# Optimization experiments

Measured on AMD Instinct MI355X. Metric: run time of the kernel, lower is better.

## Reference

```python
import jax, jax.numpy as jnp
import numpy as np

E = 256      # embed_dim
K = 8        # kNN neighbors (hard-coded in module)
B = 64       # num cells (samples)
P = 512      # objects per cell (equal segments)
N = B * P
NUM_CLASSES = 31  # 30 known + <unk> (padding idx 0)


def _normalize(x, axis=-1):
    n = jnp.linalg.norm(x, axis=axis, keepdims=True)
    return x / jnp.clip(n, 1e-12, None)


def _mlp2(x, W1, b1, W2, b2):
    # get_mlp([d_in, 64/E, d_out]): Linear-ReLU-Linear
    return jax.nn.relu(x @ W1 + b1) @ W2 + b2


def setup_inputs() -> dict:
    key = jax.random.key(0)
    ks = jax.random.split(key, 32)

    def w(k, shape, s=0.05):
        return (jax.random.normal(k, shape, jnp.float32) * s).astype(jnp.float32)

    class_table = w(ks[0], (NUM_CLASSES, E))
    class_table = class_table.at[0].set(0.0)  # padding_idx=0

    inp = {
        # learned params
        "class_table": class_table,
        "colorW1": w(ks[1], (3, 64)), "colorb1": jnp.zeros((64,), jnp.float32),
        "colorW2": w(ks[2], (64, E)), "colorb2": jnp.zeros((E,), jnp.float32),
        "posW1": w(ks[3], (3, 64)), "posb1": jnp.zeros((64,), jnp.float32),
        "posW2": w(ks[4], (64, E)), "posb2": jnp.zeros((E,), jnp.float32),
        "mergeW": w(ks[5], (3 * E, E)), "mergeb": jnp.zeros((E,), jnp.float32),
        # DynamicEdgeConv mlp: Linear(2E,E)-ReLU-BN(E)-Linear(E,E)
        "gW1": w(ks[6], (2 * E, E)), "gb1": jnp.zeros((E,), jnp.float32),
        "g_gamma": jnp.ones((E,), jnp.float32), "g_beta": jnp.zeros((E,), jnp.float32),
        "gW2": w(ks[7], (E, E)), "gb2": jnp.zeros((E,), jnp.float32),
        # final lin: Linear(E,E)-ReLU-Linear(E,E)
        "lW1": w(ks[8], (E, E)), "lb1": jnp.zeros((E,), jnp.float32),
        "lW2": w(ks[9], (E, E)), "lb2": jnp.zeros((E,), jnp.float32),
        # forward inputs
        "positions": jax.random.normal(ks[10], (N, 3), jnp.float32),
        "colors": jax.random.uniform(ks[11], (N, 3), jnp.float32),
        "class_indices": jax.random.randint(ks[12], (N,), 0, NUM_CLASSES, jnp.int64),
        "num_samples": B,
    }
    return inp


def reference(class_table, colorW1, colorb1, colorW2, colorb2,
              posW1, posb1, posW2, posb2, mergeW, mergeb,
              gW1, gb1, g_gamma, g_beta, gW2, gb2,
              lW1, lb1, lW2, lb2,
              positions, colors, class_indices, num_samples):
    # --- per-object embeddings, each L2-normalized, then merged ---
    ce = _normalize(class_table[class_indices])                         # [N,E]
    co = _normalize(_mlp2(colors, colorW1, colorb1, colorW2, colorb2))  # [N,E]
    pe = _normalize(_mlp2(positions, posW1, posb1, posW2, posb2))       # [N,E]
    emb = jnp.concatenate([ce, co, pe], axis=-1) @ mergeW + mergeb      # [N,E]

    # --- DynamicEdgeConv (variation 0): per-sample kNN in feature space ---
    x = emb.reshape(num_samples, -1, E)                                 # [B,P,E]
    sq = jnp.sum(x * x, axis=-1)                                        # [B,P]
    dist = sq[:, :, None] + sq[:, None, :] - 2.0 * jnp.einsum('bpe,bqe->bpq', x, x)
    _, idx = jax.lax.top_k(-dist, K)                                    # [B,P,K] (incl. self)

    x_nb = jax.vmap(lambda xb, ib: xb[ib])(x, idx)                      # [B,P,K,E]
    x_i = jnp.broadcast_to(x[:, :, None, :], x_nb.shape)
    msg_in = jnp.concatenate([x_i, x_nb - x_i], axis=-1)                # [B,P,K,2E]
    h = jax.nn.relu(msg_in @ gW1 + gb1)
    h = h * g_gamma + g_beta          # BatchNorm1d eval mode (running mean 0, var 1)
    h = h @ gW2 + gb2                                                   # [B,P,K,E]
    x1 = jnp.max(h, axis=2)                                             # max aggr -> [B,P,E]

    # --- global max pool over objects, final MLP, L2 normalize ---
    pooled = jnp.max(x1, axis=1)                                        # [B,E]
    out = _mlp2(pooled, lW1, lb1, lW2, lb2)
    return _normalize(out, axis=-1)
```

## Files before the change

kernel.cpp:

```cpp
#include <hip/hip_runtime.h>

#define EDIM 256
#define KNN 8
#define NB 64
#define NP 512
#define NTOT (NB * NP)

typedef short s16x8 __attribute__((ext_vector_type(8)));
typedef float f32x4 __attribute__((ext_vector_type(4)));
typedef float f32x16 __attribute__((ext_vector_type(16)));
typedef unsigned short ushort;
typedef unsigned long long u64;

__device__ __forceinline__ ushort f2b(float f) {
    unsigned u = __float_as_uint(f);
    u = (u + 0x7fffu + ((u >> 16) & 1u)) >> 16;
    return (ushort)u;
}
__device__ __forceinline__ float b2f(ushort h) {
    return __uint_as_float(((unsigned)h) << 16);
}
__device__ __forceinline__ void split2(float x, ushort& h, ushort& l) {
    h = f2b(x);
    l = f2b(x - b2f(h));
}

__device__ __forceinline__ unsigned fkey(float f) {
    const unsigned b = __float_as_uint(f);
    return (b & 0x80000000u) ? ~b : (b | 0x80000000u);
}

__device__ __forceinline__ void ins8(u64* k, u64 x) {
    #pragma unroll
    for (int j = 7; j >= 1; --j)
        k[j] = (x < k[j - 1]) ? k[j - 1] : ((x < k[j]) ? x : k[j]);
    k[0] = (x < k[0]) ? x : k[0];
}

__device__ __forceinline__ void gload16(const ushort* g, ushort* l) {
    __builtin_amdgcn_global_load_lds(
        (const __attribute__((address_space(1))) void*)g,
        (__attribute__((address_space(3))) void*)l, 16, 0, 0);
}

__global__ __launch_bounds__(256)
void k_prep(const float* __restrict__ gW1, const float* __restrict__ gW2,
            const float* __restrict__ g_gamma, const float* __restrict__ g_beta,
            const float* __restrict__ gb2,
            const float* __restrict__ cW2, const float* __restrict__ pW2,
            const float* __restrict__ cb2, const float* __restrict__ pb2,
            const float* __restrict__ mW, const float* __restrict__ ct,
            ushort* __restrict__ Wdh, ushort* __restrict__ Wdl,
            ushort* __restrict__ Wbh, ushort* __restrict__ Wbl,
            ushort* __restrict__ g2h, ushort* __restrict__ g2l,
            float* __restrict__ hb,
            ushort* __restrict__ cW2Th, ushort* __restrict__ cW2Tl,
            ushort* __restrict__ pW2Th, ushort* __restrict__ pW2Tl,
            ushort* __restrict__ WcTh, ushort* __restrict__ WcTl,
            ushort* __restrict__ WpTh, ushort* __restrict__ WpTl,
            float* __restrict__ cbM, float* __restrict__ pbM,
            float* __restrict__ classMn)
{
    __shared__ float ctn[256];
    __shared__ float red[4];
    const int bid = blockIdx.x, t = threadIdx.x;
    ushort h, l;

    if (bid < 897) {
        const int gid = bid * 256 + t;
        if (gid < 65536) {
            const int n = gid >> 8, k = gid & 255;
            split2(gW1[k * 256 + n] - gW1[(k + 256) * 256 + n], h, l);
            Wdh[gid] = h; Wdl[gid] = l;
        } else if (gid < 131072) {
            const int i = gid - 65536, n = i >> 8, k = i & 255;
            split2(gW1[(k + 256) * 256 + n], h, l);
            Wbh[i] = h; Wbl[i] = l;
        } else if (gid < 196608) {
            const int i = gid - 131072, n = i >> 8, k = i & 255;
            split2(g_gamma[k] * gW2[k * 256 + n], h, l);
            g2h[i] = h; g2l[i] = l;
        } else if (gid < 196864) {
            const int n = gid - 196608;
            float s = gb2[n];
            for (int k = 0; k < 256; ++k) s += g_beta[k] * gW2[k * 256 + n];
            hb[n] = s;
        } else if (gid < 213248) {
            const int i = gid - 196864, n = i >> 6, k = i & 63;
            split2(cW2[k * 256 + n], h, l);
            cW2Th[i] = h; cW2Tl[i] = l;
        } else if (gid < 229632) {
            const int i = gid - 213248, n = i >> 6, k = i & 63;
            split2(pW2[k * 256 + n], h, l);
            pW2Th[i] = h; pW2Tl[i] = l;
        }
        return;
    }
    if (bid < 1027) {
        const int gid = (bid - 897) * 256 + t;
        if (gid < 16384) {
            const int j = gid >> 8, n = gid & 255;
            float s = 0.f;
            for (int k = 0; k < 256; ++k) s += cW2[j * 256 + k] * mW[(256 + k) * 256 + n];
            split2(s, h, l);
            WcTh[n * 64 + j] = h; WcTl[n * 64 + j] = l;
        } else if (gid < 32768) {
            const int i = gid - 16384, j = i >> 8, n = i & 255;
            float s = 0.f;
            for (int k = 0; k < 256; ++k) s += pW2[j * 256 + k] * mW[(512 + k) * 256 + n];
            split2(s, h, l);
            WpTh[n * 64 + j] = h; WpTl[n * 64 + j] = l;
        } else if (gid < 33024) {
            const int n = gid - 32768;
            float s = 0.f;
            for (int k = 0; k < 256; ++k) s += cb2[k] * mW[(256 + k) * 256 + n];
            cbM[n] = s;
        } else if (gid < 33280) {
            const int n = gid - 33024;
            float s = 0.f;
            for (int k = 0; k < 256; ++k) s += pb2[k] * mW[(512 + k) * 256 + n];
            pbM[n] = s;
        }
        return;
    }
    {
        const int c = bid - 1027;
        const float v = ct[c * 256 + t];
        float ss = v * v;
        #pragma unroll
        for (int s = 32; s > 0; s >>= 1) ss += __shfl_down(ss, s, 64);
        if ((t & 63) == 0) red[t >> 6] = ss;
        __syncthreads();
        const float tot = red[0] + red[1] + red[2] + red[3];
        const float r = 1.f / fmaxf(sqrtf(tot), 1e-12f);
        ctn[t] = v * r;
        __syncthreads();
        float s = 0.f;
        for (int k = 0; k < 256; ++k) s += ctn[k] * mW[k * 256 + t];
        classMn[c * 256 + t] = s;
    }
}

__global__ __launch_bounds__(256)
void k_embed(const float* __restrict__ classMn,
             const float* __restrict__ cW1, const float* __restrict__ cb1,
             const float* __restrict__ cb2,
             const float* __restrict__ pW1, const float* __restrict__ pb1,
             const float* __restrict__ pb2,
             const float* __restrict__ mb,
             const ushort* __restrict__ cW2Th, const ushort* __restrict__ cW2Tl,
             const ushort* __restrict__ pW2Th, const ushort* __restrict__ pW2Tl,
             const ushort* __restrict__ WcTh, const ushort* __restrict__ WcTl,
             const ushort* __restrict__ WpTh, const ushort* __restrict__ WpTl,
             const float* __restrict__ cbM, const float* __restrict__ pbM,
             const float* __restrict__ positions, const float* __restrict__ colors,
             const int* __restrict__ cls, const int cstride,
             ushort* __restrict__ ehi, ushort* __restrict__ elo,
             float* __restrict__ sqn)
{
    __shared__ __align__(16) ushort Ahc[16 * 72];
    __shared__ __align__(16) ushort Alc[16 * 72];
    __shared__ __align__(16) ushort Ahp[16 * 72];
    __shared__ __align__(16) ushort Alp[16 * 72];
    __shared__ float sqc[16][4], sqp_[16][4], sqe[16][4];

    const int t = threadIdx.x, w = t >> 6, lane = t & 63;
    const int l15 = lane & 15, quad = lane >> 4;
    const int obase = blockIdx.x * 16;

    {
        const int o = lane >> 4;
        const int objl = w * 4 + o;
        const int gobj = obase + objl;
        const float c0 = colors[gobj * 3], c1 = colors[gobj * 3 + 1], c2 = colors[gobj * 3 + 2];
        const float q0 = positions[gobj * 3], q1 = positions[gobj * 3 + 1], q2 = positions[gobj * 3 + 2];
        const int u0 = (lane & 15) * 4;
        #pragma unroll
        for (int uu = 0; uu < 4; ++uu) {
            const int u = u0 + uu;
            const float hc = fmaxf(cb1[u] + c0 * cW1[u] + c1 * cW1[64 + u] + c2 * cW1[128 + u], 0.f);
            const float hp = fmaxf(pb1[u] + q0 * pW1[u] + q1 * pW1[64 + u] + q2 * pW1[128 + u], 0.f);
            ushort h, l;
            split2(hc, h, l); Ahc[objl * 72 + u] = h; Alc[objl * 72 + u] = l;
            split2(hp, h, l); Ahp[objl * 72 + u] = h; Alp[objl * 72 + u] = l;
        }
    }
    __syncthreads();

    f32x4 aco[4], ape[4];
    #pragma unroll
    for (int nt = 0; nt < 4; ++nt) { aco[nt] = (f32x4){0.f,0.f,0.f,0.f}; ape[nt] = (f32x4){0.f,0.f,0.f,0.f}; }

    #pragma unroll
    for (int kt = 0; kt < 2; ++kt) {
        const int ao = l15 * 72 + kt * 32 + quad * 8;
        const s16x8 ahc = *(const s16x8*)&Ahc[ao];
        const s16x8 alc = *(const s16x8*)&Alc[ao];
        const s16x8 ahp = *(const s16x8*)&Ahp[ao];
        const s16x8 alp = *(const s16x8*)&Alp[ao];
        #pragma unroll
        for (int nt = 0; nt < 4; ++nt) {
            const int n = w * 64 + nt * 16 + l15;
            const size_t bo = (size_t)n * 64 + kt * 32 + quad * 8;
            const s16x8 cbh = *(const s16x8*)(cW2Th + bo);
            const s16x8 cbl = *(const s16x8*)(cW2Tl + bo);
            const s16x8 pbh = *(const s16x8*)(pW2Th + bo);
            const s16x8 pbl = *(const s16x8*)(pW2Tl + bo);
            aco[nt] = __builtin_amdgcn_mfma_f32_16x16x32_bf16(ahc, cbh, aco[nt], 0, 0, 0);
            ape[nt] = __builtin_amdgcn_mfma_f32_16x16x32_bf16(ahp, pbh, ape[nt], 0, 0, 0);
            aco[nt] = __builtin_amdgcn_mfma_f32_16x16x32_bf16(alc, cbh, aco[nt], 0, 0, 0);
            ape[nt] = __builtin_amdgcn_mfma_f32_16x16x32_bf16(alp, pbh, ape[nt], 0, 0, 0);
            aco[nt] = __builtin_amdgcn_mfma_f32_16x16x32_bf16(ahc, cbl, aco[nt], 0, 0, 0);
            ape[nt] = __builtin_amdgcn_mfma_f32_16x16x32_bf16(ahp, pbl, ape[nt], 0, 0, 0);
        }
    }

    float sc[4] = {0.f,0.f,0.f,0.f}, sp[4] = {0.f,0.f,0.f,0.f};
    #pragma unroll
    for (int nt = 0; nt < 4; ++nt) {
        const int col = w * 64 + nt * 16 + l15;
        const float cbv = cb2[col], pbv = pb2[col];
        #pragma unroll
        for (int r = 0; r < 4; ++r) {
            const float co = aco[nt][r] + cbv;
            const float pe = ape[nt][r] + pbv;
            sc[r] += co * co;
            sp[r] += pe * pe;
        }
    }
    #pragma unroll
    for (int s = 8; s > 0; s >>= 1) {
        #pragma unroll
        for (int r = 0; r < 4; ++r) {
            sc[r] += __shfl_xor(sc[r], s, 64);
            sp[r] += __shfl_xor(sp[r], s, 64);
        }
    }
    if (l15 == 0) {
        #pragma unroll
        for (int r = 0; r < 4; ++r) { sqc[quad * 4 + r][w] = sc[r]; sqp_[quad * 4 + r][w] = sp[r]; }
    }
    __syncthreads();

    float rco[4], rpe[4];
    #pragma unroll
    for (int r = 0; r < 4; ++r) {
        const int row = quad * 4 + r;
        rco[r] = 1.f / fmaxf(sqrtf(sqc[row][0] + sqc[row][1] + sqc[row][2] + sqc[row][3]), 1e-12f);
        rpe[r] = 1.f / fmaxf(sqrtf(sqp_[row][0] + sqp_[row][1] + sqp_[row][2] + sqp_[row][3]), 1e-12f);
    }

    f32x4 ac[4], ap[4];
    #pragma unroll
    for (int nt = 0; nt < 4; ++nt) { ac[nt] = (f32x4){0.f,0.f,0.f,0.f}; ap[nt] = (f32x4){0.f,0.f,0.f,0.f}; }

    #pragma unroll
    for (int kt = 0; kt < 2; ++kt) {
        const int ao = l15 * 72 + kt * 32 + quad * 8;
        const s16x8 ahc = *(const s16x8*)&Ahc[ao];
        const s16x8 alc = *(const s16x8*)&Alc[ao];
        const s16x8 ahp = *(const s16x8*)&Ahp[ao];
        const s16x8 alp = *(const s16x8*)&Alp[ao];
        #pragma unroll
        for (int nt = 0; nt < 4; ++nt) {
            const int n = w * 64 + nt * 16 + l15;
            const size_t bo = (size_t)n * 64 + kt * 32 + quad * 8;
            const s16x8 cbh = *(const s16x8*)(WcTh + bo);
            const s16x8 cbl = *(const s16x8*)(WcTl + bo);
            const s16x8 pbh = *(const s16x8*)(WpTh + bo);
            const s16x8 pbl = *(const s16x8*)(WpTl + bo);
            ac[nt] = __builtin_amdgcn_mfma_f32_16x16x32_bf16(ahc, cbh, ac[nt], 0, 0, 0);
            ap[nt] = __builtin_amdgcn_mfma_f32_16x16x32_bf16(ahp, pbh, ap[nt], 0, 0, 0);
            ac[nt] = __builtin_amdgcn_mfma_f32_16x16x32_bf16(alc, cbh, ac[nt], 0, 0, 0);
            ap[nt] = __builtin_amdgcn_mfma_f32_16x16x32_bf16(alp, pbh, ap[nt], 0, 0, 0);
            ac[nt] = __builtin_amdgcn_mfma_f32_16x16x32_bf16(ahc, cbl, ac[nt], 0, 0, 0);
            ap[nt] = __builtin_amdgcn_mfma_f32_16x16x32_bf16(ahp, pbl, ap[nt], 0, 0, 0);
        }
    }

    int ci[4];
    #pragma unroll
    for (int r = 0; r < 4; ++r) {
        const int gobj = obase + quad * 4 + r;
        int c = cls[(size_t)gobj * cstride];
        if ((unsigned)c > 30u) c = 0;
        ci[r] = c;
    }

    float rp[4] = {0.f,0.f,0.f,0.f};
    #pragma unroll
    for (int nt = 0; nt < 4; ++nt) {
        const int col = w * 64 + nt * 16 + l15;
        const float mbv = mb[col], cbMv = cbM[col], pbMv = pbM[col];
        #pragma unroll
        for (int r = 0; r < 4; ++r) {
            const int row = quad * 4 + r;
            const float e = classMn[ci[r] * 256 + col]
                          + rco[r] * (ac[nt][r] + cbMv)
                          + rpe[r] * (ap[nt][r] + pbMv) + mbv;
            ushort h, l;
            split2(e, h, l);
            ehi[(size_t)(obase + row) * 256 + col] = h;
            elo[(size_t)(obase + row) * 256 + col] = l;
            rp[r] += e * e;
        }
    }
    #pragma unroll
    for (int s = 8; s > 0; s >>= 1) {
        #pragma unroll
        for (int r = 0; r < 4; ++r) rp[r] += __shfl_xor(rp[r], s, 64);
    }
    if (l15 == 0) {
        #pragma unroll
        for (int r = 0; r < 4; ++r) sqe[quad * 4 + r][w] = rp[r];
    }
    __syncthreads();
    if (t < 16) sqn[obase + t] = sqe[t][0] + sqe[t][1] + sqe[t][2] + sqe[t][3];
}

__global__ __launch_bounds__(256)
void k_gram(const ushort* __restrict__ ehi, const ushort* __restrict__ elo,
            const float* __restrict__ sqn, u64* __restrict__ cand)
{
    __shared__ __align__(16) ushort lds[2][4][4096];

    const int t = threadIdx.x, w = t >> 6, lane = t & 63;
    const int l15 = lane & 15, quad = lane >> 4;
    const int b = blockIdx.x;
    const int xcd = b & 7, rest = b >> 3;
    const int cell = xcd * 8 + rest / 10;
    const int tt = rest % 10;
    const int ti = (tt < 4) ? 0 : (tt < 7) ? 1 : (tt < 9) ? 2 : 3;
    const int tbase = (ti == 0) ? 0 : (ti == 1) ? 4 : (ti == 2) ? 7 : 9;
    const int tj = ti + (tt - tbase);
    const int p0 = ti * 128, q0 = tj * 128;
    const size_t cb = (size_t)cell * NP;
    const int diag = (ti == tj);
    const int wr = w >> 1, wc = w & 1;

    int srow[2], scol[2];
    #pragma unroll
    for (int i = 0; i < 2; ++i) {
        const int p = (w * 2 + i) * 64 + lane;
        const int row = p >> 2;
        srow[i] = row;
        scol[i] = ((p & 3) ^ ((row >> 1) & 3)) * 8;
    }

    #define STAGE(KT, D)                                                         \
    {                                                                            \
        const int kb_ = (KT) * 32;                                               \
        _Pragma("unroll")                                                        \
        for (int i = 0; i < 2; ++i) {                                            \
            const int ls_ = (w * 2 + i) * 512;               \
            const size_t ga_ = (cb + p0 + srow[i]) * 256 + kb_ + scol[i];        \
            gload16(ehi + ga_, &lds[D][0][ls_]);                                 \
            gload16(elo + ga_, &lds[D][1][ls_]);                                 \
            if (!diag) {                                                         \
                const size_t gq_ = (cb + q0 + srow[i]) * 256 + kb_ + scol[i];    \
                gload16(ehi + gq_, &lds[D][2][ls_]);                             \
                gload16(elo + gq_, &lds[D][3][ls_]);                             \
            }                                                                    \
        }                                                                        \
    }

    f32x4 acc[4][4];
    #pragma unroll
    for (int mt = 0; mt < 4; ++mt)
        #pragma unroll
        for (int nt = 0; nt < 4; ++nt) acc[mt][nt] = (f32x4){0.f, 0.f, 0.f, 0.f};

    const int bB = diag ? 0 : 2;

    STAGE(0, 0);
    __syncthreads();

    for (int kt = 0; kt < 8; ++kt) {
        const int cur = kt & 1;
        if (kt < 7) STAGE(kt + 1, cur ^ 1);

        s16x8 ah[4], al[4];
        #pragma unroll
        for (int mt = 0; mt < 4; ++mt) {
            const int r = wr * 64 + mt * 16 + l15;
            const int slot = 4 * r + (quad ^ ((r >> 1) & 3));
            ah[mt] = *(const s16x8*)&lds[cur][0][slot * 8];
            al[mt] = *(const s16x8*)&lds[cur][1][slot * 8];
        }
        #pragma unroll
        for (int nt = 0; nt < 4; ++nt) {
            const int rq = wc * 64 + nt * 16 + l15;
            const int slot = 4 * rq + (quad ^ ((rq >> 1) & 3));
            const s16x8 bh = *(const s16x8*)&lds[cur][bB][slot * 8];
            const s16x8 bl = *(const s16x8*)&lds[cur][bB + 1][slot * 8];
            #pragma unroll
            for (int mt = 0; mt < 4; ++mt) {
                acc[mt][nt] = __builtin_amdgcn_mfma_f32_16x16x32_bf16(ah[mt], bh, acc[mt][nt], 0, 0, 0);
                acc[mt][nt] = __builtin_amdgcn_mfma_f32_16x16x32_bf16(al[mt], bh, acc[mt][nt], 0, 0, 0);
                acc[mt][nt] = __builtin_amdgcn_mfma_f32_16x16x32_bf16(ah[mt], bl, acc[mt][nt], 0, 0, 0);
            }
        }
        __syncthreads();
    }
    #undef STAGE

    float sqp[4][4];
    #pragma unroll
    for (int mt = 0; mt < 4; ++mt)
        #pragma unroll
        for (int r = 0; r < 4; ++r)
            sqp[mt][r] = sqn[cb + p0 + wr * 64 + mt * 16 + quad * 4 + r];

    float* T = (float*)&lds[0][0][0];

    #pragma unroll
    for (int nt = 0; nt < 4; ++nt) {
        const int cq_l = wc * 64 + nt * 16 + l15;
        const float sq_q = sqn[cb + q0 + cq_l];
        #pragma unroll
        for (int mt = 0; mt < 4; ++mt) {
            #pragma unroll
            for (int r = 0; r < 4; ++r) {
                const int rp_l = wr * 64 + mt * 16 + quad * 4 + r;
                const float d = (sqp[mt][r] + sq_q) - 2.f * acc[mt][nt][r];
                T[rp_l * 128 + (cq_l ^ rp_l)] = d;
            }
        }
    }
    __syncthreads();

    {
        const int row = t >> 1, half = t & 1;

        u64 k8[8];
        #pragma unroll
        for (int j = 0; j < 8; ++j) k8[j] = ~0ull;
        for (int c = 0; c < 64; ++c) {
            const int cc = half * 64 + c;
            const float f = T[row * 128 + (cc ^ row)];
            ins8(k8, ((u64)fkey(f) << 32) | (unsigned)(q0 + cc));
        }
        {
            u64 part[8];
            #pragma unroll
            for (int j = 0; j < 8; ++j) part[j] = __shfl_xor(k8[j], 1, 64);
            #pragma unroll
            for (int j = 0; j < 8; ++j) ins8(k8, part[j]);
        }
        if (half == 0) {
            u64* cp = cand + ((size_t)(cb + p0 + row)) * 32 + tj * 8;
            #pragma unroll
            for (int j = 0; j < 8; ++j) cp[j] = k8[j];
        }

        if (!diag) {
            u64 q8[8];
            #pragma unroll
            for (int j = 0; j < 8; ++j) q8[j] = ~0ull;
            for (int c = 0; c < 64; ++c) {
                const int rr = half * 64 + c;
                const float f = T[rr * 128 + (row ^ rr)];
                ins8(q8, ((u64)fkey(f) << 32) | (unsigned)(p0 + rr));
            }
            {
                u64 part[8];
                #pragma unroll
                for (int j = 0; j < 8; ++j) part[j] = __shfl_xor(q8[j], 1, 64);
                #pragma unroll
                for (int j = 0; j < 8; ++j) ins8(q8, part[j]);
            }
            if (half == 0) {
                u64* cp = cand + ((size_t)(cb + q0 + row)) * 32 + ti * 8;
                #pragma unroll
                for (int j = 0; j < 8; ++j) cp[j] = q8[j];
            }
        }
    }
}

__global__ __launch_bounds__(256)
void k_nidx(const u64* __restrict__ cand, int* __restrict__ nidx)
{
    const int p = blockIdx.x * 256 + threadIdx.x;
    const u64* cp = cand + (size_t)p * 32;
    u64 k8[8];
    #pragma unroll
    for (int j = 0; j < 8; ++j) k8[j] = ~0ull;
    #pragma unroll
    for (int i = 0; i < 32; ++i) ins8(k8, cp[i]);
    const int hi = (p >> 9) << 9;
    #pragma unroll
    for (int r = 0; r < 8; ++r)
        nidx[(size_t)p * KNN + r] = hi | (int)(k8[r] & 0x1ffu);
}

__global__ __launch_bounds__(256)
void k_uv(const ushort* __restrict__ ehi, const ushort* __restrict__ elo,
          const ushort* __restrict__ Wdh, const ushort* __restrict__ Wbh,
          const float* __restrict__ gb1,
          float* __restrict__ u, float* __restrict__ v)
{
    (void)elo;
    __shared__ __align__(16) ushort lds[2][2048];

    const int t = threadIdx.x, w = t >> 6, lane = t & 63;
    const int l15 = lane & 15, quad = lane >> 4;
    const int isV = blockIdx.x >> 9;
    const int m0 = (blockIdx.x & 511) * 64;
    const ushort* Wh = isV ? Wbh : Wdh;
    float* out = isV ? v : u;
    const int mh = w & 1, ch = w >> 1;

    const int sp = w * 64 + lane;
    const int srow = sp >> 2;
    const int scol = ((sp & 3) ^ ((srow >> 1) & 3)) * 8;

    #define STAGE_UV(S, D)                                                       \
    {                                                                            \
        const size_t ga_ = (size_t)(m0 + srow) * 256 + (S) * 32 + scol;          \
        gload16(ehi + ga_, &lds[D][sp * 8]);                                     \
    }

    const int r0 = mh * 32 + l15, r1 = r0 + 16;
    const int slot0 = 4 * r0 + (quad ^ ((r0 >> 1) & 3));
    const int slot1 = 4 * r1 + (quad ^ ((r1 >> 1) & 3));

    f32x4 acc[2][8];
    #pragma unroll
    for (int mt = 0; mt < 2; ++mt)
        #pragma unroll
        for (int nt = 0; nt < 8; ++nt) acc[mt][nt] = (f32x4){0.f, 0.f, 0.f, 0.f};

    STAGE_UV(0, 0);
    __syncthreads();

    for (int s = 0; s < 8; ++s) {
        const int cur = s & 1;
        if (s < 7) STAGE_UV(s + 1, cur ^ 1);

        const s16x8 ah0 = *(const s16x8*)&lds[cur][slot0 * 8];
        const s16x8 ah1 = *(const s16x8*)&lds[cur][slot1 * 8];
        #pragma unroll
        for (int nt = 0; nt < 8; ++nt) {
            const int n = ch * 128 + nt * 16 + l15;
            const size_t bo = (size_t)n * 256 + s * 32 + quad * 8;
            const s16x8 bh = *(const s16x8*)(Wh + bo);
            acc[0][nt] = __builtin_amdgcn_mfma_f32_16x16x32_bf16(ah0, bh, acc[0][nt], 0, 0, 0);
            acc[1][nt] = __builtin_amdgcn_mfma_f32_16x16x32_bf16(ah1, bh, acc[1][nt], 0, 0, 0);
        }
        __syncthreads();
    }
    #undef STAGE_UV

    #pragma unroll
    for (int mt = 0; mt < 2; ++mt) {
        #pragma unroll
        for (int nt = 0; nt < 8; ++nt) {
            const int col = ch * 128 + nt * 16 + l15;
            const float bias = isV ? 0.f : gb1[col];
            #pragma unroll
            for (int r = 0; r < 4; ++r) {
                const int row = mh * 32 + mt * 16 + quad * 4 + r;
                out[(size_t)(m0 + row) * 256 + col] = acc[mt][nt][r] + bias;
            }
        }
    }
}

__global__ __launch_bounds__(512)
void k_edge(const float* __restrict__ u, const float* __restrict__ v,
            const int* __restrict__ nidx,
            const ushort* __restrict__ g2h,
            const float* __restrict__ hb,
            float* __restrict__ part)
{
    __shared__ ushort Abuf[2][2304];
    __shared__ float ustage[2048];

    const int t = threadIdx.x, w = t >> 6, lane = t & 63;
    const int l31 = lane & 31, kh = lane >> 5;

    const int b = blockIdx.x;
    const int xcd = b & 7, rest = b >> 3;
    const int cell = xcd * 8 + (rest >> 6);
    const int pl0 = cell * NP + (rest & 63) * 8;

    {
        const int pt = t >> 6, kk = (t & 63) * 4;
        *(float4*)&ustage[pt * 256 + kk] = *(const float4*)(u + (size_t)(pl0 + pt) * 256 + kk);
    }

    const int se = t >> 3, kq = t & 7;
    const int upt = se >> 3;
    int svrow = nidx[(size_t)(pl0 + upt) * KNN + (se & 7)];
    if ((unsigned)svrow >= (unsigned)NTOT) svrow = 0;

    __syncthreads();

    float4 vr[2];

    #define VLOAD(S)                                                             \
    {                                                                            \
        const int k0 = (S) * 32 + kq * 4;                                        \
        vr[(S) & 1] = *(const float4*)(v + (size_t)svrow * 256 + k0);            \
    }
    #define SPLITW(S, BUF)                                                       \
    {                                                                            \
        const int k0u = (S) * 32 + kq * 4;                                       \
        const float4 ua = *(const float4*)&ustage[upt * 256 + k0u];              \
        const float4 va = vr[(S) & 1];                                           \
        const float sv[4] = {                                                    \
            fmaxf(ua.x + va.x, 0.f), fmaxf(ua.y + va.y, 0.f),                    \
            fmaxf(ua.z + va.z, 0.f), fmaxf(ua.w + va.w, 0.f)};                   \
        union { uint2 q; ushort us[4]; } th;                                     \
        _Pragma("unroll")                                                        \
        for (int j = 0; j < 4; ++j) { th.us[j] = f2b(sv[j]); }                   \
        *(uint2*)&Abuf[BUF][se * 36 + kq * 4] = th.q;                            \
    }

    #define LDS_BARRIER()                                                        \
    {                                                                            \
        asm volatile("s_waitcnt lgkmcnt(0)" ::: "memory");                       \
        __builtin_amdgcn_s_barrier();                                            \
    }

    f32x16 acc[2];
    acc[0] = (f32x16)(0.0f);
    acc[1] = (f32x16)(0.0f);

    VLOAD(0); VLOAD(1);
    SPLITW(0, 0);

    #pragma unroll
    for (int s = 0; s < 8; ++s) {
        LDS_BARRIER();
        if (s < 7) {
            SPLITW(s + 1, (s + 1) & 1);
            if (s < 6) VLOAD(s + 2);
        }

        s16x8 ah[2][2];
        #pragma unroll
        for (int mt = 0; mt < 2; ++mt) {
            #pragma unroll
            for (int kc = 0; kc < 2; ++kc) {
                const int ao = (mt * 32 + l31) * 36 + kc * 16 + kh * 8;
                union { uint2 q[2]; s16x8 v8; } Th;
                Th.q[0] = *(const uint2*)&Abuf[s & 1][ao];
                Th.q[1] = *(const uint2*)&Abuf[s & 1][ao + 4];
                ah[mt][kc] = Th.v8;
            }
        }

        #pragma unroll
        for (int kc = 0; kc < 2; ++kc) {
            const int n = w * 32 + l31;
            const s16x8 bh = *(const s16x8*)(g2h + (size_t)n * 256 + s * 32 + kc * 16 + kh * 8);
            acc[0] = __builtin_amdgcn_mfma_f32_32x32x16_bf16(ah[0][kc], bh, acc[0], 0, 0, 0);
            acc[1] = __builtin_amdgcn_mfma_f32_32x32x16_bf16(ah[1][kc], bh, acc[1], 0, 0, 0);
        }
    }
    #undef VLOAD
    #undef SPLITW
    #undef LDS_BARRIER

    const int slot = rest & 63;
    {
        float rm = -3.4e38f;
        #pragma unroll
        for (int r = 0; r < 16; ++r)
            rm = fmaxf(rm, fmaxf(acc[0][r], acc[1][r]));
        rm = fmaxf(rm, __shfl_xor(rm, 32, 64));
        if (kh == 0) {
            const int col = w * 32 + l31;
            part[((size_t)cell * 64 + slot) * 256 + col] = rm + hb[col];
        }
    }
}

__global__ __launch_bounds__(256)
void k_final(const float* __restrict__ part,
             const float* __restrict__ lW1, const float* __restrict__ lb1,
             const float* __restrict__ lW2, const float* __restrict__ lb2,
             float* __restrict__ out)
{
    __shared__ float pooled[256];
    __shared__ float hid[256];
    __shared__ float red[4];

    const int b = blockIdx.x;
    const int t = threadIdx.x;

    float m = -3.4e38f;
    for (int s = 0; s < 64; ++s)
        m = fmaxf(m, part[((size_t)b * 64 + s) * 256 + t]);
    pooled[t] = m;
    __syncthreads();

    float h = lb1[t];
    for (int k = 0; k < 256; k += 4) {
        #pragma unroll
        for (int kk = 0; kk < 4; ++kk)
            h += pooled[k + kk] * lW1[(k + kk) * 256 + t];
    }
    hid[t] = fmaxf(h, 0.f);
    __syncthreads();

    float o = lb2[t];
    for (int k = 0; k < 256; k += 4) {
        #pragma unroll
        for (int kk = 0; kk < 4; ++kk)
            o += hid[k + kk] * lW2[(k + kk) * 256 + t];
    }

    float ss = o * o;
    #pragma unroll
    for (int s = 32; s > 0; s >>= 1) ss += __shfl_down(ss, s, 64);
    if ((t & 63) == 0) red[t >> 6] = ss;
    __syncthreads();
    const float tot = red[0] + red[1] + red[2] + red[3];
    const float rn = 1.f / fmaxf(sqrtf(tot), 1e-12f);
    out[b * 256 + t] = o * rn;
}

extern "C" void kernel_launch(void* const* d_in, const int* in_sizes, int n_in,
                              void* d_out, int out_size, void* d_ws, size_t ws_size,
                              hipStream_t stream)
{
    (void)n_in; (void)out_size; (void)ws_size;

    const float* class_table = (const float*)d_in[0];
    const float* cW1 = (const float*)d_in[1];
    const float* cb1 = (const float*)d_in[2];
    const float* cW2 = (const float*)d_in[3];
    const float* cb2 = (const float*)d_in[4];
    const float* pW1 = (const float*)d_in[5];
    const float* pb1 = (const float*)d_in[6];
    const float* pW2 = (const float*)d_in[7];
    const float* pb2 = (const float*)d_in[8];
    const float* mW  = (const float*)d_in[9];
    const float* mb  = (const float*)d_in[10];
    const float* gW1 = (const float*)d_in[11];
    const float* gb1 = (const float*)d_in[12];
    const float* g_gamma = (const float*)d_in[13];
    const float* g_beta  = (const float*)d_in[14];
    const float* gW2 = (const float*)d_in[15];
    const float* gb2 = (const float*)d_in[16];
    const float* lW1 = (const float*)d_in[17];
    const float* lb1 = (const float*)d_in[18];
    const float* lW2 = (const float*)d_in[19];
    const float* lb2 = (const float*)d_in[20];
    const float* positions = (const float*)d_in[21];
    const float* colors    = (const float*)d_in[22];
    const int*  cls        = (const int*)d_in[23];

    const int cstride = (in_sizes[23] == 2 * NTOT) ? 2 : 1;

    char* base = (char*)d_ws;
    float*   part   = (float*)(base + 0);
    ushort*  Wdh    = (ushort*)(base + 4194304);
    ushort*  Wdl    = (ushort*)(base + 4325376);
    ushort*  Wbh    = (ushort*)(base + 4456448);
    ushort*  Wbl    = (ushort*)(base + 4587520);
    ushort*  g2h    = (ushort*)(base + 4718592);
    ushort*  g2l    = (ushort*)(base + 4849664);
    float*   hb     = (float*)(base + 4980736);
    ushort*  cW2Th  = (ushort*)(base + 4981760);
    ushort*  cW2Tl  = (ushort*)(base + 5014528);
    ushort*  pW2Th  = (ushort*)(base + 5047296);
    ushort*  pW2Tl  = (ushort*)(base + 5080064);
    ushort*  WcTh   = (ushort*)(base + 5112832);
    ushort*  WcTl   = (ushort*)(base + 5145600);
    ushort*  WpTh   = (ushort*)(base + 5178368);
    ushort*  WpTl   = (ushort*)(base + 5211136);
    float*   classMn= (float*)(base + 5243904);
    float*   cbM    = (float*)(base + 5275648);
    float*   pbM    = (float*)(base + 5276672);
    int*     nidx   = (int*)(base + 5277696);
    float*   sqn    = (float*)(base + 6326272);
    ushort*  ehi    = (ushort*)(base + 6457344);
    ushort*  elo    = (ushort*)(base + 23234560);
    u64*     cand   = (u64*)(base + 40011776);
    float*   v      = (float*)(base + 107120640);
    float*   u      = (float*)(base + 140675072);
    float* out = (float*)d_out;

    k_prep<<<1058, 256, 0, stream>>>(gW1, gW2, g_gamma, g_beta, gb2, cW2, pW2,
                                     cb2, pb2, mW, class_table,
                                     Wdh, Wdl, Wbh, Wbl, g2h, g2l, hb,
                                     cW2Th, cW2Tl, pW2Th, pW2Tl,
                                     WcTh, WcTl, WpTh, WpTl, cbM, pbM, classMn);

    k_embed<<<NTOT / 16, 256, 0, stream>>>(classMn, cW1, cb1, cb2, pW1, pb1, pb2,
                                           mb, cW2Th, cW2Tl, pW2Th, pW2Tl,
                                           WcTh, WcTl, WpTh, WpTl, cbM, pbM,
                                           positions, colors, cls, cstride,
                                           ehi, elo, sqn);
    k_gram<<<NB * 10, 256, 0, stream>>>(ehi, elo, sqn, cand);
    k_nidx<<<NTOT / 256, 256, 0, stream>>>(cand, nidx);
    k_uv<<<2 * NTOT / 64, 256, 0, stream>>>(ehi, elo, Wdh, Wbh, gb1, u, v);
    k_edge<<<NTOT / 8, 512, 0, stream>>>(u, v, nidx, g2h, hb, part);
    k_final<<<NB, 256, 0, stream>>>(part, lW1, lb1, lW2, lb2, out);
}
```

Baseline: 404.0 us.

## Merge kNN index and u/v GEMM launches; double k-step in edge kernel

Folds the k_nidx top-8 merge into the k_uv launch as 128 extra blocks, which removes one kernel launch and lets the two independent jobs overlap. In k_edge the K loop now runs 4 stages of 64 instead of 8 stages of 32. This halves the number of LDS barriers and doubles the MFMA work between them. The cost is a larger padded LDS A-buffer and more registers per thread, which may lower occupancy.

```diff
diff --git a/kernel.cpp b/kernel.cpp
--- a/kernel.cpp
+++ b/kernel.cpp
@@ -479,31 +479,32 @@
 }
 
 __global__ __launch_bounds__(256)
-void k_nidx(const u64* __restrict__ cand, int* __restrict__ nidx)
+void k_uvnidx(const ushort* __restrict__ ehi,
+              const ushort* __restrict__ Wdh, const ushort* __restrict__ Wbh,
+              const float* __restrict__ gb1,
+              float* __restrict__ u, float* __restrict__ v,
+              const u64* __restrict__ cand, int* __restrict__ nidx)
 {
-    const int p = blockIdx.x * 256 + threadIdx.x;
-    const u64* cp = cand + (size_t)p * 32;
-    u64 k8[8];
-    #pragma unroll
-    for (int j = 0; j < 8; ++j) k8[j] = ~0ull;
-    #pragma unroll
-    for (int i = 0; i < 32; ++i) ins8(k8, cp[i]);
-    const int hi = (p >> 9) << 9;
-    #pragma unroll
-    for (int r = 0; r < 8; ++r)
-        nidx[(size_t)p * KNN + r] = hi | (int)(k8[r] & 0x1ffu);
-}
-
-__global__ __launch_bounds__(256)
-void k_uv(const ushort* __restrict__ ehi, const ushort* __restrict__ elo,
-          const ushort* __restrict__ Wdh, const ushort* __restrict__ Wbh,
-          const float* __restrict__ gb1,
-          float* __restrict__ u, float* __restrict__ v)
-{
-    (void)elo;
     __shared__ __align__(16) ushort lds[2][2048];
 
-    const int t = threadIdx.x, w = t >> 6, lane = t & 63;
+    const int t = threadIdx.x;
+
+    if (blockIdx.x >= 1024) {
+        const int p = (blockIdx.x - 1024) * 256 + t;
+        const u64* cp = cand + (size_t)p * 32;
+        u64 k8[8];
+        #pragma unroll
+        for (int j = 0; j < 8; ++j) k8[j] = ~0ull;
+        #pragma unroll
+        for (int i = 0; i < 32; ++i) ins8(k8, cp[i]);
+        const int hi = (p >> 9) << 9;
+        #pragma unroll
+        for (int r = 0; r < 8; ++r)
+            nidx[(size_t)p * KNN + r] = hi | (int)(k8[r] & 0x1ffu);
+        return;
+    }
+
+    const int w = t >> 6, lane = t & 63;
     const int l15 = lane & 15, quad = lane >> 4;
     const int isV = blockIdx.x >> 9;
     const int m0 = (blockIdx.x & 511) * 64;
@@ -574,7 +575,7 @@
             const float* __restrict__ hb,
             float* __restrict__ part)
 {
-    __shared__ ushort Abuf[2][2304];
+    __shared__ ushort Abuf[2][4352];
     __shared__ float ustage[2048];
 
     const int t = threadIdx.x, w = t >> 6, lane = t & 63;
@@ -597,25 +598,30 @@
 
     __syncthreads();
 
-    float4 vr[2];
+    float4 vr[2][2];
 
     #define VLOAD(S)                                                             \
     {                                                                            \
-        const int k0 = (S) * 32 + kq * 4;                                        \
-        vr[(S) & 1] = *(const float4*)(v + (size_t)svrow * 256 + k0);            \
+        const int k0 = (S) * 64 + kq * 8;                                        \
+        vr[(S) & 1][0] = *(const float4*)(v + (size_t)svrow * 256 + k0);         \
+        vr[(S) & 1][1] = *(const float4*)(v + (size_t)svrow * 256 + k0 + 4);     \
     }
     #define SPLITW(S, BUF)                                                       \
     {                                                                            \
-        const int k0u = (S) * 32 + kq * 4;                                       \
+        const int k0u = (S) * 64 + kq * 8;                                       \
         const float4 ua = *(const float4*)&ustage[upt * 256 + k0u];              \
-        const float4 va = vr[(S) & 1];                                           \
-        const float sv[4] = {                                                    \
+        const float4 ub = *(const float4*)&ustage[upt * 256 + k0u + 4];          \
+        const float4 va = vr[(S) & 1][0], vb = vr[(S) & 1][1];                   \
+        const float sv[8] = {                                                    \
             fmaxf(ua.x + va.x, 0.f), fmaxf(ua.y + va.y, 0.f),                    \
-            fmaxf(ua.z + va.z, 0.f), fmaxf(ua.w + va.w, 0.f)};                   \
-        union { uint2 q; ushort us[4]; } th;                                     \
+            fmaxf(ua.z + va.z, 0.f), fmaxf(ua.w + va.w, 0.f),                    \
+            fmaxf(ub.x + vb.x, 0.f), fmaxf(ub.y + vb.y, 0.f),                    \
+            fmaxf(ub.z + vb.z, 0.f), fmaxf(ub.w + vb.w, 0.f)};                   \
+        union { uint2 q[2]; ushort us[8]; } th;                                  \
         _Pragma("unroll")                                                        \
-        for (int j = 0; j < 4; ++j) { th.us[j] = f2b(sv[j]); }                   \
-        *(uint2*)&Abuf[BUF][se * 36 + kq * 4] = th.q;                            \
+        for (int j = 0; j < 8; ++j) { th.us[j] = f2b(sv[j]); }                   \
+        *(uint2*)&Abuf[BUF][se * 68 + kq * 8]     = th.q[0];                     \
+        *(uint2*)&Abuf[BUF][se * 68 + kq * 8 + 4] = th.q[1];                     \
     }
 
     #define LDS_BARRIER()                                                        \
@@ -632,30 +638,30 @@
     SPLITW(0, 0);
 
     #pragma unroll
-    for (int s = 0; s < 8; ++s) {
+    for (int S = 0; S < 4; ++S) {
         LDS_BARRIER();
-        if (s < 7) {
-            SPLITW(s + 1, (s + 1) & 1);
-            if (s < 6) VLOAD(s + 2);
-        }
-
-        s16x8 ah[2][2];
+        if (S < 3) {
+            SPLITW(S + 1, (S + 1) & 1);
+            if (S < 2) VLOAD(S + 2);
+        }
+
+        s16x8 ah[2][4];
         #pragma unroll
         for (int mt = 0; mt < 2; ++mt) {
             #pragma unroll
-            for (int kc = 0; kc < 2; ++kc) {
-                const int ao = (mt * 32 + l31) * 36 + kc * 16 + kh * 8;
+            for (int kc = 0; kc < 4; ++kc) {
+                const int ao = (mt * 32 + l31) * 68 + kc * 16 + kh * 8;
                 union { uint2 q[2]; s16x8 v8; } Th;
-                Th.q[0] = *(const uint2*)&Abuf[s & 1][ao];
-                Th.q[1] = *(const uint2*)&Abuf[s & 1][ao + 4];
+                Th.q[0] = *(const uint2*)&Abuf[S & 1][ao];
+                Th.q[1] = *(const uint2*)&Abuf[S & 1][ao + 4];
                 ah[mt][kc] = Th.v8;
             }
         }
 
         #pragma unroll
-        for (int kc = 0; kc < 2; ++kc) {
+        for (int kc = 0; kc < 4; ++kc) {
             const int n = w * 32 + l31;
-            const s16x8 bh = *(const s16x8*)(g2h + (size_t)n * 256 + s * 32 + kc * 16 + kh * 8);
+            const s16x8 bh = *(const s16x8*)(g2h + (size_t)n * 256 + S * 64 + kc * 16 + kh * 8);
             acc[0] = __builtin_amdgcn_mfma_f32_32x32x16_bf16(ah[0][kc], bh, acc[0], 0, 0, 0);
             acc[1] = __builtin_amdgcn_mfma_f32_32x32x16_bf16(ah[1][kc], bh, acc[1], 0, 0, 0);
         }
@@ -797,8 +803,8 @@
                                            positions, colors, cls, cstride,
                                            ehi, elo, sqn);
     k_gram<<<NB * 10, 256, 0, stream>>>(ehi, elo, sqn, cand);
-    k_nidx<<<NTOT / 256, 256, 0, stream>>>(cand, nidx);
-    k_uv<<<2 * NTOT / 64, 256, 0, stream>>>(ehi, elo, Wdh, Wbh, gb1, u, v);
+    k_uvnidx<<<1024 + NTOT / 256, 256, 0, stream>>>(ehi, Wdh, Wbh, gb1, u, v,
+                                                    cand, nidx);
     k_edge<<<NTOT / 8, 512, 0, stream>>>(u, v, nidx, g2h, hb, part);
     k_final<<<NB, 256, 0, stream>>>(part, lW1, lb1, lW2, lb2, out);
 }
```

Measured after the change: 391.1 us. 1.03x faster.
